# Kernel optimization log

Hardware: AMD Instinct MI355X
Metric: run time of the kernel (lower is better)

Reference implementation:

```python
import jax, jax.numpy as jnp
import numpy as np
from jax import lax

BN_EPS = 1e-5
DN = ('NCHW', 'OIHW', 'NCHW')


def _bn_silu(y, s, b, m, v):
    # eval-mode BatchNorm2d followed by SiLU
    inv = s / jnp.sqrt(v + BN_EPS)
    y = y * inv[None, :, None, None] + (b - m * inv)[None, :, None, None]
    return jax.nn.silu(y)


def _dsconv(x, dw_w, pw_w, s, b, m, v):
    c = x.shape[1]
    y = lax.conv_general_dilated(x, dw_w, (1, 1), [(1, 1), (1, 1)],
                                 dimension_numbers=DN, feature_group_count=c)
    y = lax.conv_general_dilated(y, pw_w, (1, 1), [(0, 0), (0, 0)],
                                 dimension_numbers=DN)
    return _bn_silu(y, s, b, m, v)


def setup_inputs() -> dict:
    key = jax.random.key(0)
    ks = jax.random.split(key, 8)
    B, C, H, W, OUT, TOPK = 32, 256, 64, 64, 256, 2
    CS = C // 2
    inp = {
        'x': jax.random.normal(ks[0], (B, C, H, W), jnp.float32),
        'weights': jax.random.uniform(ks[1], (B, TOPK), jnp.float32),
        'indices': jax.random.randint(ks[2], (B, TOPK), 0, 4),
        'dw_w0': jax.random.normal(ks[3], (CS, 1, 3, 3), jnp.float32) * 0.1,
        'pw_w0': jax.random.normal(ks[4], (OUT, CS, 1, 1), jnp.float32) * 0.05,
        'bn0_s': jnp.ones((OUT,), jnp.float32),
        'bn0_b': jnp.zeros((OUT,), jnp.float32),
        'bn0_m': jnp.zeros((OUT,), jnp.float32),
        'bn0_v': jnp.ones((OUT,), jnp.float32),
        'dw_w1': jax.random.normal(ks[5], (CS, 1, 3, 3), jnp.float32) * 0.1,
        'pw_w1': jax.random.normal(ks[6], (OUT, CS, 1, 1), jnp.float32) * 0.05,
        'bn1_s': jnp.ones((OUT,), jnp.float32),
        'bn1_b': jnp.zeros((OUT,), jnp.float32),
        'bn1_m': jnp.zeros((OUT,), jnp.float32),
        'bn1_v': jnp.ones((OUT,), jnp.float32),
        'w2': jax.random.normal(ks[7], (OUT, C, 1, 1), jnp.float32) * 0.05,
        'bn2_s': jnp.ones((OUT,), jnp.float32),
        'bn2_b': jnp.zeros((OUT,), jnp.float32),
        'bn2_m': jnp.zeros((OUT,), jnp.float32),
        'bn2_v': jnp.ones((OUT,), jnp.float32),
    }
    return inp


def reference(x, weights, indices,
              dw_w0, pw_w0, bn0_s, bn0_b, bn0_m, bn0_v,
              dw_w1, pw_w1, bn1_s, bn1_b, bn1_m, bn1_v,
              w2, bn2_s, bn2_b, bn2_m, bn2_v):
    cs = x.shape[1] // 2
    x_rgb, x_ir = x[:, :cs], x[:, cs:]
    # Per-expert routing coefficient: sum over top-k slots of weight * (index == e).
    # Mathematically identical to the torch masked scatter-add loop.
    def coeff(e):
        return jnp.sum(weights * (indices == e).astype(weights.dtype), axis=1)  # [B]
    e0 = _dsconv(x_rgb, dw_w0, pw_w0, bn0_s, bn0_b, bn0_m, bn0_v)
    e1 = _dsconv(x_ir, dw_w1, pw_w1, bn1_s, bn1_b, bn1_m, bn1_v)
    e2 = _bn_silu(lax.conv_general_dilated(x, w2, (1, 1), [(0, 0), (0, 0)],
                                           dimension_numbers=DN),
                  bn2_s, bn2_b, bn2_m, bn2_v)
    out = (coeff(0)[:, None, None, None] * e0
           + coeff(1)[:, None, None, None] * e1
           + coeff(2)[:, None, None, None] * e2)
    return out
```

## Files before the change

kernel.cpp:

```cpp
#include <hip/hip_runtime.h>

typedef __bf16 bf16x8 __attribute__((ext_vector_type(8)));
typedef float f32x4 __attribute__((ext_vector_type(4)));

#define BN_EPS 1e-5f

__device__ __forceinline__ unsigned short f2bf(float f) {
    union { float f; unsigned u; } x; x.f = f;
    unsigned r = x.u + 0x7fffu + ((x.u >> 16) & 1u);
    return (unsigned short)(r >> 16);
}

__device__ __forceinline__ unsigned pk_bf16(float lo, float hi) {
    unsigned r;
    asm("v_cvt_pk_bf16_f32 %0, %1, %2" : "=v"(r) : "v"(lo), "v"(hi));
    return r;
}

__device__ __forceinline__ float fcomp(float4 v, int j) {
    return (j == 0) ? v.x : (j == 1) ? v.y : (j == 2) ? v.z : v.w;
}

__global__ void prep_kernel(const float* __restrict__ pw0, const float* __restrict__ pw1,
                            const float* __restrict__ w2,
                            const float* __restrict__ s0, const float* __restrict__ b0,
                            const float* __restrict__ m0, const float* __restrict__ v0,
                            const float* __restrict__ s1, const float* __restrict__ b1,
                            const float* __restrict__ m1, const float* __restrict__ v1,
                            const float* __restrict__ s2, const float* __restrict__ b2,
                            const float* __restrict__ m2, const float* __restrict__ v2,
                            unsigned short* __restrict__ wfF0, unsigned short* __restrict__ wfF1,
                            unsigned short* __restrict__ wfF2, float* __restrict__ beta) {
    int o = blockIdx.x;
    int t = threadIdx.x;
    float inv0 = s0[o] * rsqrtf(v0[o] + BN_EPS);
    float inv1 = s1[o] * rsqrtf(v1[o] + BN_EPS);
    float inv2 = s2[o] * rsqrtf(v2[o] + BN_EPS);
    if (t == 0) {
        beta[0 * 256 + o] = b0[o] - m0[o] * inv0;
        beta[1 * 256 + o] = b1[o] - m1[o] * inv1;
        beta[2 * 256 + o] = b2[o] - m2[o] * inv2;
    }
    if (t < 128) {
        wfF0[((t >> 3) * 256 + o) * 8 + (t & 7)] = f2bf(pw0[o * 128 + t] * inv0);
        wfF1[((t >> 3) * 256 + o) * 8 + (t & 7)] = f2bf(pw1[o * 128 + t] * inv1);
    }
    wfF2[((t >> 3) * 256 + o) * 8 + (t & 7)] = f2bf(w2[o * 256 + t] * inv2);
}

template<int NK>
__device__ __forceinline__ void gemm_expert(const char* lds, const unsigned short* __restrict__ W,
                                            int qb, int wave, int l15, int l4,
                                            const int* pxv, const int* swv, f32x4 acc[2][4]) {
    const int row0 = wave * 32 + l15;
#pragma unroll
    for (int ck = 0; ck < NK; ck += 4) {
        bf16x8 af[4][2];
#pragma unroll
        for (int kk = 0; kk < 4; ++kk)
#pragma unroll
            for (int ot = 0; ot < 2; ++ot)
                af[kk][ot] = *(const bf16x8*)(W + (((ck + kk) * 4 + l4) * 256 + row0 + ot * 16) * 8);
#pragma unroll
        for (int kk = 0; kk < 4; ++kk) {
            bf16x8 bb[4];
#pragma unroll
            for (int tp = 0; tp < 4; ++tp)
                bb[tp] = *(const bf16x8*)(lds + pxv[tp] * 512 + ((qb + (ck + kk) * 64 + l4 * 16) ^ swv[tp]));
#pragma unroll
            for (int ot = 0; ot < 2; ++ot)
#pragma unroll
                for (int tp = 0; tp < 4; ++tp)
                    acc[ot][tp] = __builtin_amdgcn_mfma_f32_16x16x32_bf16(af[kk][ot], bb[tp], acc[ot][tp], 0, 0, 0);
        }
    }
}

__device__ __forceinline__ void epilogue(const f32x4 acc[2][4], float ce, const float* __restrict__ bp,
                                         int wave, int l4, f32x4 res[2][4]) {
#pragma unroll
    for (int ot = 0; ot < 2; ++ot)
#pragma unroll
        for (int j = 0; j < 4; ++j) {
            const int o = wave * 32 + ot * 16 + l4 * 4 + j;
            const float bet = bp[o];
#pragma unroll
            for (int tp = 0; tp < 4; ++tp) {
                float v = acc[ot][tp][j] + bet;
                float sig = __builtin_amdgcn_rcpf(1.f + __expf(-v));
                res[ot][tp][j] += ce * (v * sig);
            }
        }
}

__global__ __launch_bounds__(512, 3)
void fused_kernel(const float* __restrict__ x,
                  const float* __restrict__ wts, const int* __restrict__ idx,
                  const float* __restrict__ dw0, const float* __restrict__ dw1,
                  const unsigned short* __restrict__ wfF0,
                  const unsigned short* __restrict__ wfF1,
                  const unsigned short* __restrict__ wfF2,
                  const float* __restrict__ beta,
                  float* __restrict__ out) {
    __shared__ __align__(16) char lds[34816];

    const int tid  = threadIdx.x;
    const int wave = tid >> 6;
    const int lane = tid & 63;

    const int bid = blockIdx.x;
    const int xcd = bid & 7;
    const int j   = bid >> 3;
    const int b   = j >> 3;
    const int h   = xcd * 8 + (j & 7);

    float c0 = 0.f, c1 = 0.f, c2 = 0.f;
#pragma unroll
    for (int t = 0; t < 2; ++t) {
        int e = idx[b * 2 + t];
        float w = wts[b * 2 + t];
        if (e == 0) c0 += w;
        else if (e == 1) c1 += w;
        else if (e == 2) c2 += w;
    }
    const bool do0 = (c0 != 0.f), do1 = (c1 != 0.f), do2 = (c2 != 0.f);

    const long rowBase = (long)b * 1048576L;

    const int g   = lane >> 2;
    const int kq  = lane & 3;
    const int px0 = g * 4;
    const int l15 = lane & 15;
    const int l4  = lane >> 4;
    const float* xb = x + rowBase + h * 64 + px0;
    const bool hm = (h > 0), hp = (h < 63);

    int pxv[4], swv[4];
#pragma unroll
    for (int tp = 0; tp < 4; ++tp) {
        pxv[tp] = tp * 16 + l15;
        swv[tp] = (pxv[tp] & 15) << 4;
    }

    if (do0 || do1) {
        if ((wave < 4) ? do0 : do1) {
            float4 RM[8], RC[8], RP[8];
            const float4 z4 = make_float4(0.f, 0.f, 0.f, 0.f);
#pragma unroll
            for (int c = 0; c < 8; ++c) {
                const int k = wave * 32 + ((c >> 2) << 4) + kq * 4 + (c & 3);
                const float* xc = xb + (long)k * 4096;
                RM[c] = hm ? *(const float4*)(xc - 64) : z4;
                RC[c] = *(const float4*)(xc);
                RP[c] = hp ? *(const float4*)(xc + 64) : z4;
            }
#pragma unroll
            for (int i = 0; i < 2; ++i) {
                const int k0 = wave * 32 + i * 16 + kq * 4;
                unsigned dw_p[2][4];
#pragma unroll
                for (int pr = 0; pr < 2; ++pr) {
                    float y[2][4];
#pragma unroll
                    for (int k2 = 0; k2 < 2; ++k2) {
                        const int c  = i * 4 + pr * 2 + k2;
                        const int k  = k0 + pr * 2 + k2;
                        const float* dwp = (k < 128) ? (dw0 + k * 9) : (dw1 + (k - 128) * 9);
                        float4 rm = RM[c], rc = RC[c], rp = RP[c];
                        float lm = __shfl_up(rm.w, 4), lc = __shfl_up(rc.w, 4), lp = __shfl_up(rp.w, 4);
                        float Rm = __shfl_down(rm.x, 4), Rc = __shfl_down(rc.x, 4), Rp = __shfl_down(rp.x, 4);
                        if (g == 0)  { lm = 0.f; lc = 0.f; lp = 0.f; }
                        if (g == 15) { Rm = 0.f; Rc = 0.f; Rp = 0.f; }
                        const float w0 = dwp[0], w1 = dwp[1], w2 = dwp[2];
                        const float w3 = dwp[3], w4 = dwp[4], w5 = dwp[5];
                        const float w6 = dwp[6], w7 = dwp[7], w8 = dwp[8];
                        y[k2][0] = w0*lm   + w1*rm.x + w2*rm.y + w3*lc   + w4*rc.x + w5*rc.y + w6*lp   + w7*rp.x + w8*rp.y;
                        y[k2][1] = w0*rm.x + w1*rm.y + w2*rm.z + w3*rc.x + w4*rc.y + w5*rc.z + w6*rp.x + w7*rp.y + w8*rp.z;
                        y[k2][2] = w0*rm.y + w1*rm.z + w2*rm.w + w3*rc.y + w4*rc.z + w5*rc.w + w6*rp.y + w7*rp.z + w8*rp.w;
                        y[k2][3] = w0*rm.z + w1*rm.w + w2*Rm   + w3*rc.z + w4*rc.w + w5*Rc   + w6*rp.z + w7*rp.w + w8*Rp;
                    }
#pragma unroll
                    for (int j2 = 0; j2 < 4; ++j2)
                        dw_p[pr][j2] = pk_bf16(y[0][j2], y[1][j2]);
                }
                const int colb = (k0 >> 3) * 16;
                const int sub  = (k0 & 4) * 2;
#pragma unroll
                for (int j2 = 0; j2 < 4; ++j2) {
                    const int px = px0 + j2;
                    *(uint2*)(lds + px * 512 + ((colb ^ ((px & 15) << 4))) + sub) =
                        make_uint2(dw_p[0][j2], dw_p[1][j2]);
                }
            }
        }
        __syncthreads();
    }

    f32x4 res[2][4];
#pragma unroll
    for (int ot = 0; ot < 2; ++ot)
#pragma unroll
        for (int tp = 0; tp < 4; ++tp)
            res[ot][tp] = (f32x4){0.f, 0.f, 0.f, 0.f};

    if (do0 || do1) {
        if (do0) {
            f32x4 acc[2][4];
#pragma unroll
            for (int ot = 0; ot < 2; ++ot)
#pragma unroll
                for (int tp = 0; tp < 4; ++tp) acc[ot][tp] = (f32x4){0.f, 0.f, 0.f, 0.f};
            gemm_expert<4>(lds, wfF0, 0, wave, l15, l4, pxv, swv, acc);
            epilogue(acc, c0, beta, wave, l4, res);
        }
        if (do1) {
            f32x4 acc[2][4];
#pragma unroll
            for (int ot = 0; ot < 2; ++ot)
#pragma unroll
                for (int tp = 0; tp < 4; ++tp) acc[ot][tp] = (f32x4){0.f, 0.f, 0.f, 0.f};
            gemm_expert<4>(lds, wfF1, 256, wave, l15, l4, pxv, swv, acc);
            epilogue(acc, c1, beta + 256, wave, l4, res);
        }
    }

    if (do2) {
        __syncthreads();
        {
            const int cb = wave * 32 + kq * 8;
            float4 r[8];
#pragma unroll
            for (int c = 0; c < 8; ++c)
                r[c] = *(const float4*)(xb + (long)(cb + c) * 4096);
            const int colb = (cb >> 3) * 16;
#pragma unroll
            for (int j2 = 0; j2 < 4; ++j2) {
                const int px = px0 + j2;
                float v0 = fcomp(r[0], j2), v1 = fcomp(r[1], j2), v2 = fcomp(r[2], j2), v3 = fcomp(r[3], j2);
                float v4 = fcomp(r[4], j2), v5 = fcomp(r[5], j2), v6 = fcomp(r[6], j2), v7 = fcomp(r[7], j2);
                *(uint4*)(lds + px * 512 + ((colb ^ ((px & 15) << 4)))) =
                    make_uint4(pk_bf16(v0, v1), pk_bf16(v2, v3), pk_bf16(v4, v5), pk_bf16(v6, v7));
            }
        }
        __syncthreads();
        {
            f32x4 acc[2][4];
#pragma unroll
            for (int ot = 0; ot < 2; ++ot)
#pragma unroll
                for (int tp = 0; tp < 4; ++tp) acc[ot][tp] = (f32x4){0.f, 0.f, 0.f, 0.f};
            gemm_expert<8>(lds, wfF2, 0, wave, l15, l4, pxv, swv, acc);
            epilogue(acc, c2, beta + 512, wave, l4, res);
        }
    }

    float* lf = (float*)lds;
    const long outB = rowBase + h * 64;
    __syncthreads();
#pragma unroll
    for (int r = 0; r < 2; ++r) {
        if ((wave >> 2) == r) {
#pragma unroll
            for (int ot = 0; ot < 2; ++ot)
#pragma unroll
                for (int j2 = 0; j2 < 4; ++j2) {
                    const int o = wave * 32 + ot * 16 + l4 * 4 + j2;
#pragma unroll
                    for (int tp = 0; tp < 4; ++tp)
                        lf[(o & 127) * 68 + tp * 16 + l15] = res[ot][tp][j2];
                }
        }
        __syncthreads();
        {
            const int rowq = tid >> 3;
            const int col  = (tid & 7) * 8;
#pragma unroll
            for (int rr = 0; rr < 2; ++rr) {
                const int lr = rowq + rr * 64;
                float4 v0 = *(float4*)&lf[lr * 68 + col];
                float4 v1 = *(float4*)&lf[lr * 68 + col + 4];
                float* op = out + outB + (long)(r * 128 + lr) * 4096 + col;
                *(float4*)op = v0;
                *(float4*)(op + 4) = v1;
            }
        }
        __syncthreads();
    }
}

extern "C" void kernel_launch(void* const* d_in, const int* in_sizes, int n_in,
                              void* d_out, int out_size, void* d_ws, size_t ws_size,
                              hipStream_t stream) {
    const float* x    = (const float*)d_in[0];
    const float* wts  = (const float*)d_in[1];
    const int*   idx  = (const int*)d_in[2];
    const float* dw0  = (const float*)d_in[3];
    const float* pw0  = (const float*)d_in[4];
    const float* s0   = (const float*)d_in[5];
    const float* b0   = (const float*)d_in[6];
    const float* m0   = (const float*)d_in[7];
    const float* v0   = (const float*)d_in[8];
    const float* dw1  = (const float*)d_in[9];
    const float* pw1  = (const float*)d_in[10];
    const float* s1   = (const float*)d_in[11];
    const float* b1   = (const float*)d_in[12];
    const float* m1   = (const float*)d_in[13];
    const float* v1   = (const float*)d_in[14];
    const float* w2   = (const float*)d_in[15];
    const float* s2   = (const float*)d_in[16];
    const float* b2   = (const float*)d_in[17];
    const float* m2   = (const float*)d_in[18];
    const float* v2   = (const float*)d_in[19];

    char* ws = (char*)d_ws;
    unsigned short* wfF0 = (unsigned short*)ws;
    unsigned short* wfF1 = (unsigned short*)(ws + 65536);
    unsigned short* wfF2 = (unsigned short*)(ws + 131072);
    float*          beta = (float*)(ws + 262144);

    prep_kernel<<<256, 256, 0, stream>>>(pw0, pw1, w2,
                                         s0, b0, m0, v0,
                                         s1, b1, m1, v1,
                                         s2, b2, m2, v2,
                                         wfF0, wfF1, wfF2, beta);

    fused_kernel<<<2048, 512, 0, stream>>>(x, wts, idx, dw0, dw1,
                                           wfF0, wfF1, wfF2, beta, (float*)d_out);
}
```

Before: 82.88 us.

## Stage raw and depthwise tiles in separate LDS regions from one x load

The LDS buffer is doubled so the depthwise-conv output for experts 0/1 and the raw bf16 tile for expert 2 are staged in separate regions. Both are produced from a single pass of global loads of the center rows, so x is no longer reloaded for expert 2. Two barriers are removed and the expert 2 GEMM reads from the second region. The cost is doubled LDS per block (about 68KB), which may lower occupancy at the 512-thread, 3-blocks launch bound.

```diff
diff --git a/kernel.cpp b/kernel.cpp
--- a/kernel.cpp
+++ b/kernel.cpp
@@ -102,7 +102,7 @@
                   const unsigned short* __restrict__ wfF2,
                   const float* __restrict__ beta,
                   float* __restrict__ out) {
-    __shared__ __align__(16) char lds[34816];
+    __shared__ __align__(16) char lds[69632];
 
     const int tid  = threadIdx.x;
     const int wave = tid >> 6;
@@ -142,29 +142,32 @@
         swv[tp] = (pxv[tp] & 15) << 4;
     }
 
-    if (do0 || do1) {
-        if ((wave < 4) ? do0 : do1) {
-            float4 RM[8], RC[8], RP[8];
-            const float4 z4 = make_float4(0.f, 0.f, 0.f, 0.f);
-#pragma unroll
-            for (int c = 0; c < 8; ++c) {
-                const int k = wave * 32 + ((c >> 2) << 4) + kq * 4 + (c & 3);
-                const float* xc = xb + (long)k * 4096;
+    const bool dwact = (wave < 4) ? do0 : do1;
+    if (dwact || do2) {
+        float4 RM[8], RC[8], RP[8];
+        const float4 z4 = make_float4(0.f, 0.f, 0.f, 0.f);
+#pragma unroll
+        for (int c = 0; c < 8; ++c) {
+            const int k = wave * 32 + ((c >> 2) << 4) + kq * 4 + (c & 3);
+            const float* xc = xb + (long)k * 4096;
+            RC[c] = *(const float4*)(xc);
+            if (dwact) {
                 RM[c] = hm ? *(const float4*)(xc - 64) : z4;
-                RC[c] = *(const float4*)(xc);
                 RP[c] = hp ? *(const float4*)(xc + 64) : z4;
             }
-#pragma unroll
-            for (int i = 0; i < 2; ++i) {
-                const int k0 = wave * 32 + i * 16 + kq * 4;
-                unsigned dw_p[2][4];
-#pragma unroll
-                for (int pr = 0; pr < 2; ++pr) {
-                    float y[2][4];
-#pragma unroll
-                    for (int k2 = 0; k2 < 2; ++k2) {
-                        const int c  = i * 4 + pr * 2 + k2;
-                        const int k  = k0 + pr * 2 + k2;
+        }
+#pragma unroll
+        for (int i = 0; i < 2; ++i) {
+            const int k0 = wave * 32 + i * 16 + kq * 4;
+            unsigned dw_p[2][4], rw_p[2][4];
+#pragma unroll
+            for (int pr = 0; pr < 2; ++pr) {
+                float y[2][4];
+#pragma unroll
+                for (int k2 = 0; k2 < 2; ++k2) {
+                    const int c = i * 4 + pr * 2 + k2;
+                    const int k = k0 + pr * 2 + k2;
+                    if (dwact) {
                         const float* dwp = (k < 128) ? (dw0 + k * 9) : (dw1 + (k - 128) * 9);
                         float4 rm = RM[c], rc = RC[c], rp = RP[c];
                         float lm = __shfl_up(rm.w, 4), lc = __shfl_up(rc.w, 4), lp = __shfl_up(rp.w, 4);
@@ -179,22 +182,33 @@
                         y[k2][2] = w0*rm.y + w1*rm.z + w2*rm.w + w3*rc.y + w4*rc.z + w5*rc.w + w6*rp.y + w7*rp.z + w8*rp.w;
                         y[k2][3] = w0*rm.z + w1*rm.w + w2*Rm   + w3*rc.z + w4*rc.w + w5*Rc   + w6*rp.z + w7*rp.w + w8*Rp;
                     }
+                }
+                if (dwact) {
 #pragma unroll
                     for (int j2 = 0; j2 < 4; ++j2)
                         dw_p[pr][j2] = pk_bf16(y[0][j2], y[1][j2]);
                 }
-                const int colb = (k0 >> 3) * 16;
-                const int sub  = (k0 & 4) * 2;
-#pragma unroll
-                for (int j2 = 0; j2 < 4; ++j2) {
-                    const int px = px0 + j2;
-                    *(uint2*)(lds + px * 512 + ((colb ^ ((px & 15) << 4))) + sub) =
-                        make_uint2(dw_p[0][j2], dw_p[1][j2]);
+                if (do2) {
+                    const int c0i = i * 4 + pr * 2;
+#pragma unroll
+                    for (int j2 = 0; j2 < 4; ++j2)
+                        rw_p[pr][j2] = pk_bf16(fcomp(RC[c0i], j2), fcomp(RC[c0i + 1], j2));
                 }
             }
-        }
-        __syncthreads();
-    }
+            const int colb = (k0 >> 3) * 16;
+            const int sub  = (k0 & 4) * 2;
+#pragma unroll
+            for (int j2 = 0; j2 < 4; ++j2) {
+                const int px  = px0 + j2;
+                const int off = px * 512 + ((colb ^ ((px & 15) << 4))) + sub;
+                if (dwact)
+                    *(uint2*)(lds + off) = make_uint2(dw_p[0][j2], dw_p[1][j2]);
+                if (do2)
+                    *(uint2*)(lds + 32768 + off) = make_uint2(rw_p[0][j2], rw_p[1][j2]);
+            }
+        }
+    }
+    __syncthreads();
 
     f32x4 res[2][4];
 #pragma unroll
@@ -203,55 +217,32 @@
         for (int tp = 0; tp < 4; ++tp)
             res[ot][tp] = (f32x4){0.f, 0.f, 0.f, 0.f};
 
-    if (do0 || do1) {
-        if (do0) {
-            f32x4 acc[2][4];
-#pragma unroll
-            for (int ot = 0; ot < 2; ++ot)
-#pragma unroll
-                for (int tp = 0; tp < 4; ++tp) acc[ot][tp] = (f32x4){0.f, 0.f, 0.f, 0.f};
-            gemm_expert<4>(lds, wfF0, 0, wave, l15, l4, pxv, swv, acc);
-            epilogue(acc, c0, beta, wave, l4, res);
-        }
-        if (do1) {
-            f32x4 acc[2][4];
-#pragma unroll
-            for (int ot = 0; ot < 2; ++ot)
-#pragma unroll
-                for (int tp = 0; tp < 4; ++tp) acc[ot][tp] = (f32x4){0.f, 0.f, 0.f, 0.f};
-            gemm_expert<4>(lds, wfF1, 256, wave, l15, l4, pxv, swv, acc);
-            epilogue(acc, c1, beta + 256, wave, l4, res);
-        }
-    }
-
+    if (do0) {
+        f32x4 acc[2][4];
+#pragma unroll
+        for (int ot = 0; ot < 2; ++ot)
+#pragma unroll
+            for (int tp = 0; tp < 4; ++tp) acc[ot][tp] = (f32x4){0.f, 0.f, 0.f, 0.f};
+        gemm_expert<4>(lds, wfF0, 0, wave, l15, l4, pxv, swv, acc);
+        epilogue(acc, c0, beta, wave, l4, res);
+    }
+    if (do1) {
+        f32x4 acc[2][4];
+#pragma unroll
+        for (int ot = 0; ot < 2; ++ot)
+#pragma unroll
+            for (int tp = 0; tp < 4; ++tp) acc[ot][tp] = (f32x4){0.f, 0.f, 0.f, 0.f};
+        gemm_expert<4>(lds, wfF1, 256, wave, l15, l4, pxv, swv, acc);
+        epilogue(acc, c1, beta + 256, wave, l4, res);
+    }
     if (do2) {
-        __syncthreads();
-        {
-            const int cb = wave * 32 + kq * 8;
-            float4 r[8];
-#pragma unroll
-            for (int c = 0; c < 8; ++c)
-                r[c] = *(const float4*)(xb + (long)(cb + c) * 4096);
-            const int colb = (cb >> 3) * 16;
-#pragma unroll
-            for (int j2 = 0; j2 < 4; ++j2) {
-                const int px = px0 + j2;
-                float v0 = fcomp(r[0], j2), v1 = fcomp(r[1], j2), v2 = fcomp(r[2], j2), v3 = fcomp(r[3], j2);
-                float v4 = fcomp(r[4], j2), v5 = fcomp(r[5], j2), v6 = fcomp(r[6], j2), v7 = fcomp(r[7], j2);
-                *(uint4*)(lds + px * 512 + ((colb ^ ((px & 15) << 4)))) =
-                    make_uint4(pk_bf16(v0, v1), pk_bf16(v2, v3), pk_bf16(v4, v5), pk_bf16(v6, v7));
-            }
-        }
-        __syncthreads();
-        {
-            f32x4 acc[2][4];
-#pragma unroll
-            for (int ot = 0; ot < 2; ++ot)
-#pragma unroll
-                for (int tp = 0; tp < 4; ++tp) acc[ot][tp] = (f32x4){0.f, 0.f, 0.f, 0.f};
-            gemm_expert<8>(lds, wfF2, 0, wave, l15, l4, pxv, swv, acc);
-            epilogue(acc, c2, beta + 512, wave, l4, res);
-        }
+        f32x4 acc[2][4];
+#pragma unroll
+        for (int ot = 0; ot < 2; ++ot)
+#pragma unroll
+            for (int tp = 0; tp < 4; ++tp) acc[ot][tp] = (f32x4){0.f, 0.f, 0.f, 0.f};
+        gemm_expert<8>(lds + 32768, wfF2, 0, wave, l15, l4, pxv, swv, acc);
+        epilogue(acc, c2, beta + 512, wave, l4, res);
     }
 
     float* lf = (float*)lds;
```

Measured after the change: 106.8 us. +28.9%, slower.
